# Optimization experiments

Measured on AMD Instinct MI355X. Metric: run time of the kernel, lower is better.

## Reference

```python
import jax, jax.numpy as jnp
import numpy as np

B = 32768
W = 7            # window_size (fixed: classifier head outputs 7*2 -> view(B, 7, 2))
F = 80           # per-frame feature size
WF = W * F       # window_feature_size = 560
EH = 512         # encoder_hidden_size
EO = 512         # encoder_output_size
H = 512          # core_hidden_size
NUM_STEPS = 7
EPS = 1e-5

def _linear(x, w, b):
    return x @ w.T + b

def _bn(x, g, bt, m, v):
    # BatchNorm1d in eval mode (running stats)
    return (x - m) * g / jnp.sqrt(v + EPS) + bt

def _ln(x, g, b):
    mu = x.mean(-1, keepdims=True)
    var = x.var(-1, keepdims=True)
    return (x - mu) / jnp.sqrt(var + EPS) * g + b

def setup_inputs():
    key = jax.random.key(0)
    ks = iter(jax.random.split(key, 40))
    def rn(shape, s=0.05):
        return jax.random.normal(next(ks), shape, dtype=jnp.float32) * s
    def rv(shape):
        return jax.random.uniform(next(ks), shape, dtype=jnp.float32) + 0.5
    return {
        'features': jax.random.normal(next(ks), (B, W, F), dtype=jnp.float32),
        'dec_w': rn((W, H)), 'dec_b': rn((W,)),
        'dec_bn_g': rv((W,)), 'dec_bn_b': rn((W,)), 'dec_bn_m': rn((W,)), 'dec_bn_v': rv((W,)),
        'ea1_w': rn((EH, W)), 'ea1_b': rn((EH,)),
        'ea1_bn_g': rv((EH,)), 'ea1_bn_b': rn((EH,)), 'ea1_bn_m': rn((EH,)), 'ea1_bn_v': rv((EH,)),
        'ea2_w': rn((EO, EH)), 'ea2_b': rn((EO,)),
        'ea2_bn_g': rv((EO,)), 'ea2_bn_b': rn((EO,)), 'ea2_bn_m': rn((EO,)), 'ea2_bn_v': rv((EO,)),
        'ei1_w': rn((EH, WF)), 'ei1_b': rn((EH,)),
        'ei1_bn_g': rv((EH,)), 'ei1_bn_b': rn((EH,)), 'ei1_bn_m': rn((EH,)), 'ei1_bn_v': rv((EH,)),
        'ei2_w': rn((EO, EH)), 'ei2_b': rn((EO,)),
        'ei2_bn_g': rv((EO,)), 'ei2_bn_b': rn((EO,)), 'ei2_bn_m': rn((EO,)), 'ei2_bn_v': rv((EO,)),
        'w_ih': rn((4 * H, EO)), 'w_hh': rn((4 * H, H)), 'b_ih': rn((4 * H,)), 'b_hh': rn((4 * H,)),
        'ln_g': rv((H,)), 'ln_b': rn((H,)),
        'cls_w': rn((2 * W, H)), 'cls_b': rn((2 * W,)),
    }

def _forward(features, dec_w, dec_b, dec_bn_g, dec_bn_b, dec_bn_m, dec_bn_v,
             ea1_w, ea1_b, ea1_bn_g, ea1_bn_b, ea1_bn_m, ea1_bn_v,
             ea2_w, ea2_b, ea2_bn_g, ea2_bn_b, ea2_bn_m, ea2_bn_v,
             ei1_w, ei1_b, ei1_bn_g, ei1_bn_b, ei1_bn_m, ei1_bn_v,
             ei2_w, ei2_b, ei2_bn_g, ei2_bn_b, ei2_bn_m, ei2_bn_v,
             w_ih, w_hh, b_ih, b_hh, ln_g, ln_b, cls_w, cls_b):
    Bsz = features.shape[0]

    def encoder(att):
        # attention branch: Linear -> BN -> ReLU -> Linear -> BN
        a = jax.nn.relu(_bn(_linear(att, ea1_w, ea1_b), ea1_bn_g, ea1_bn_b, ea1_bn_m, ea1_bn_v))
        a = _bn(_linear(a, ea2_w, ea2_b), ea2_bn_g, ea2_bn_b, ea2_bn_m, ea2_bn_v)
        # attended-input branch on flattened (features * att)
        ai = (features * att[:, :, None]).reshape(Bsz, WF)
        x = jax.nn.relu(_bn(_linear(ai, ei1_w, ei1_b), ei1_bn_g, ei1_bn_b, ei1_bn_m, ei1_bn_v))
        x = _bn(_linear(x, ei2_w, ei2_b), ei2_bn_g, ei2_bn_b, ei2_bn_m, ei2_bn_v)
        return jax.nn.relu(a + x)

    def lstm_step(x, h, c):
        gates = x @ w_ih.T + b_ih + h @ w_hh.T + b_hh  # [B, 4H], torch gate order i,f,g,o
        i, f, g, o = jnp.split(gates, 4, axis=-1)
        c = jax.nn.sigmoid(f) * c + jax.nn.sigmoid(i) * jnp.tanh(g)
        h = jax.nn.sigmoid(o) * jnp.tanh(c)
        return h, c

    # initial pass: uniform attention, zero LSTM state (state=None -> no LN)
    att0 = jnp.full((Bsz, W), 1.0 / W, dtype=features.dtype)
    h, c = lstm_step(encoder(att0), jnp.zeros((Bsz, H), features.dtype), jnp.zeros((Bsz, H), features.dtype))

    def body(carry, _):
        h, c = carry
        # decoder: Linear -> BN -> smooth softmax
        logits = _bn(_linear(h, dec_w, dec_b), dec_bn_g, dec_bn_b, dec_bn_m, dec_bn_v)
        s = jax.nn.sigmoid(logits)
        att = s / s.sum(-1, keepdims=True)
        agg = encoder(att)
        hn, cn = lstm_step(agg, _ln(h, ln_g, ln_b), _ln(c, ln_g, ln_b))
        return (hn, cn), None

    (h, c), _ = jax.lax.scan(body, (h, c), None, length=NUM_STEPS)
    out = _linear(h, cls_w, cls_b).reshape(Bsz, W, 2)
    return jax.nn.log_softmax(out, axis=2)

def reference(features, dec_w, dec_b, dec_bn_g, dec_bn_b, dec_bn_m, dec_bn_v,
              ea1_w, ea1_b, ea1_bn_g, ea1_bn_b, ea1_bn_m, ea1_bn_v,
              ea2_w, ea2_b, ea2_bn_g, ea2_bn_b, ea2_bn_m, ea2_bn_v,
              ei1_w, ei1_b, ei1_bn_g, ei1_bn_b, ei1_bn_m, ei1_bn_v,
              ei2_w, ei2_b, ei2_bn_g, ei2_bn_b, ei2_bn_m, ei2_bn_v,
              w_ih, w_hh, b_ih, b_hh, ln_g, ln_b, cls_w, cls_b):
    return _forward(features, dec_w, dec_b, dec_bn_g, dec_bn_b, dec_bn_m, dec_bn_v,
                    ea1_w, ea1_b, ea1_bn_g, ea1_bn_b, ea1_bn_m, ea1_bn_v,
                    ea2_w, ea2_b, ea2_bn_g, ea2_bn_b, ea2_bn_m, ea2_bn_v,
                    ei1_w, ei1_b, ei1_bn_g, ei1_bn_b, ei1_bn_m, ei1_bn_v,
                    ei2_w, ei2_b, ei2_bn_g, ei2_bn_b, ei2_bn_m, ei2_bn_v,
                    w_ih, w_hh, b_ih, b_hh, ln_g, ln_b, cls_w, cls_b)
```

## Files before the change

kernel.cpp:

```cpp
#include <hip/hip_runtime.h>
#include <cstdint>
#include <cstddef>

#define BSZ 32768
#define WN 7
#define WF 560
#define K1P 576
#define EPS 1e-5f

typedef __attribute__((ext_vector_type(8))) short bf16x8;
typedef __attribute__((ext_vector_type(4))) float f32x4;

__device__ __forceinline__ float b2f(short s) {
  union { float f; unsigned u; } x; x.u = ((unsigned)(unsigned short)s) << 16; return x.f;
}
__device__ __forceinline__ short f2b(float f) {
  union { float f; unsigned u; } x; x.f = f;
  unsigned r = x.u + 0x7fffu + ((x.u >> 16) & 1u);
  return (short)(r >> 16);
}
__device__ __forceinline__ float sigf(float x) { return 1.0f / (1.0f + __expf(-x)); }
__device__ __forceinline__ float ftanh(float x) {
  float t = __expf(-2.0f * fabsf(x));
  float r = (1.0f - t) / (1.0f + t);
  return copysignf(r, x);
}

__device__ __forceinline__ void async_copy16(const short* g, short* l) {
  __builtin_amdgcn_global_load_lds((const __attribute__((address_space(1))) unsigned*)g,
                                   (__attribute__((address_space(3))) unsigned*)l, 16, 0, 0);
}


__global__ void fold_small_k(const float* __restrict__ dec_w, const float* __restrict__ dec_b,
                             const float* __restrict__ dec_g, const float* __restrict__ dec_bt,
                             const float* __restrict__ dec_m, const float* __restrict__ dec_v,
                             const float* __restrict__ ea1_w, const float* __restrict__ ea1_b,
                             const float* __restrict__ ea1_g, const float* __restrict__ ea1_bt,
                             const float* __restrict__ ea1_m, const float* __restrict__ ea1_v,
                             float* __restrict__ decwf, float* __restrict__ decb8,
                             float* __restrict__ ea1f)
{
  int t = blockIdx.x * 256 + threadIdx.x;
  if (t < 7 * 512) {
    int w = t >> 9;
    float s = dec_g[w] * rsqrtf(dec_v[w] + EPS);
    decwf[t] = dec_w[t] * s;
  }
  if (t < 8) {
    if (t < 7) {
      float s = dec_g[t] * rsqrtf(dec_v[t] + EPS);
      decb8[t] = (dec_b[t] - dec_m[t]) * s + dec_bt[t];
    } else decb8[t] = 0.0f;
  }
  if (t < 512) {
    float s = ea1_g[t] * rsqrtf(ea1_v[t] + EPS);
    #pragma unroll
    for (int w = 0; w < 7; ++w) ea1f[t * 8 + w] = ea1_w[t * 7 + w] * s;
    ea1f[t * 8 + 7] = (ea1_b[t] - ea1_m[t]) * s + ea1_bt[t];
  }
}

__global__ void fold_ei1_k(const float* __restrict__ w, const float* __restrict__ b,
                           const float* __restrict__ g, const float* __restrict__ bt,
                           const float* __restrict__ m, const float* __restrict__ v,
                           short* __restrict__ ei1f, float* __restrict__ bias1)
{
  int idx = blockIdx.x * 256 + threadIdx.x;
  int n = idx / K1P, k = idx % K1P;
  float s = g[n] * rsqrtf(v[n] + EPS);
  ei1f[idx] = (k < WF) ? f2b(w[n * WF + k] * s) : (short)0;
  if (k == 0) bias1[n] = (b[n] - m[n]) * s + bt[n];
}

__global__ void fold_w2_k(const float* __restrict__ wi, const float* __restrict__ bi,
                          const float* __restrict__ gi, const float* __restrict__ bti,
                          const float* __restrict__ mi, const float* __restrict__ vi,
                          const float* __restrict__ wa, const float* __restrict__ ba,
                          const float* __restrict__ ga, const float* __restrict__ bta,
                          const float* __restrict__ ma, const float* __restrict__ va,
                          short* __restrict__ W2, float* __restrict__ bias2)
{
  int idx = blockIdx.x * 256 + threadIdx.x;
  int n = idx >> 10, k = idx & 1023;
  float si = gi[n] * rsqrtf(vi[n] + EPS);
  float sa = ga[n] * rsqrtf(va[n] + EPS);
  float val = (k < 512) ? wi[n * 512 + k] * si : wa[n * 512 + (k - 512)] * sa;
  W2[idx] = f2b(val);
  if (k == 0)
    bias2[n] = (bi[n] - mi[n]) * si + bti[n] + (ba[n] - ma[n]) * sa + bta[n];
}

__global__ void fold_wg_k(const float* __restrict__ w_ih, const float* __restrict__ w_hh,
                          const float* __restrict__ b_ih, const float* __restrict__ b_hh,
                          short* __restrict__ Wg, float* __restrict__ biasg)
{
  int idx = blockIdx.x * 256 + threadIdx.x;
  int c = idx >> 10, k = idx & 1023;
  int g = (c >> 4) & 3;
  int u = (c >> 6) * 16 + (c & 15);
  int r = g * 512 + u;
  float val = (k < 512) ? w_ih[r * 512 + k] : w_hh[r * 512 + (k - 512)];
  Wg[idx] = f2b(val);
  if (k == 0) biasg[c] = b_ih[r] + b_hh[r];
}

__global__ __launch_bounds__(512)
void attln_k(const float* __restrict__ hbuf, const float* __restrict__ cbuf,
             const float* __restrict__ decwf, const float* __restrict__ decb8,
             const float* __restrict__ ea1f,
             const float* __restrict__ ln_g, const float* __restrict__ ln_b,
             const float* __restrict__ feat,
             short* __restrict__ ghA, short* __restrict__ c_ln,
             short* __restrict__ xa, short* __restrict__ ai, int init)
{
  const int lane = threadIdx.x & 63;
  const int b = blockIdx.x * 8 + (threadIdx.x >> 6);
  float av[WN];
  if (init) {
    const float c7 = 1.0f / 7.0f;
    #pragma unroll
    for (int w = 0; w < WN; ++w) av[w] = c7;
    int4 z = make_int4(0, 0, 0, 0);
    *(int4*)&ghA[b * 1024 + 512 + lane * 8] = z;
    *(int4*)&c_ln[b * 512 + lane * 8] = z;
  } else {
    float hl[8];
    const float* hp = hbuf + (size_t)b * 512 + lane * 8;
    *(float4*)&hl[0] = *(const float4*)hp;
    *(float4*)&hl[4] = *(const float4*)(hp + 4);
    float s = 0.f, s2 = 0.f;
    #pragma unroll
    for (int e = 0; e < 8; ++e) { s += hl[e]; s2 += hl[e] * hl[e]; }
    float p[WN];
    #pragma unroll
    for (int w = 0; w < WN; ++w) {
      const float* dw = decwf + w * 512 + lane * 8;
      float4 w0 = *(const float4*)dw, w1 = *(const float4*)(dw + 4);
      p[w] = hl[0] * w0.x + hl[1] * w0.y + hl[2] * w0.z + hl[3] * w0.w
           + hl[4] * w1.x + hl[5] * w1.y + hl[6] * w1.z + hl[7] * w1.w;
    }
    #pragma unroll
    for (int o = 32; o > 0; o >>= 1) {
      s  += __shfl_xor(s, o);
      s2 += __shfl_xor(s2, o);
      #pragma unroll
      for (int w = 0; w < WN; ++w) p[w] += __shfl_xor(p[w], o);
    }
    float mu = s * (1.0f / 512.0f);
    float var = s2 * (1.0f / 512.0f) - mu * mu;
    float rstd = rsqrtf(var + EPS);
    float ssum = 0.f;
    #pragma unroll
    for (int w = 0; w < WN; ++w) { float sg = sigf(p[w] + decb8[w]); av[w] = sg; ssum += sg; }
    float inv = 1.0f / ssum;
    #pragma unroll
    for (int w = 0; w < WN; ++w) av[w] *= inv;
    short o8[8];
    #pragma unroll
    for (int e = 0; e < 8; ++e) {
      int i = lane * 8 + e;
      o8[e] = f2b((hl[e] - mu) * rstd * ln_g[i] + ln_b[i]);
    }
    *(int4*)&ghA[b * 1024 + 512 + lane * 8] = *(int4*)o8;
    float cl[8];
    const float* cp = cbuf + (size_t)b * 512 + lane * 8;
    *(float4*)&cl[0] = *(const float4*)cp;
    *(float4*)&cl[4] = *(const float4*)(cp + 4);
    float cs = 0.f, cs2 = 0.f;
    #pragma unroll
    for (int e = 0; e < 8; ++e) { cs += cl[e]; cs2 += cl[e] * cl[e]; }
    #pragma unroll
    for (int o = 32; o > 0; o >>= 1) {
      cs  += __shfl_xor(cs, o);
      cs2 += __shfl_xor(cs2, o);
    }
    float cmu = cs * (1.0f / 512.0f);
    float cvar = cs2 * (1.0f / 512.0f) - cmu * cmu;
    float crstd = rsqrtf(cvar + EPS);
    #pragma unroll
    for (int e = 0; e < 8; ++e) {
      int i = lane * 8 + e;
      o8[e] = f2b((cl[e] - cmu) * crstd * ln_g[i] + ln_b[i]);
    }
    *(int4*)&c_ln[b * 512 + lane * 8] = *(int4*)o8;
  }
  short a8[8];
  #pragma unroll
  for (int e = 0; e < 8; ++e) {
    int n = lane * 8 + e;
    const float* wr = ea1f + n * 8;
    float4 w0 = *(const float4*)wr, w1 = *(const float4*)(wr + 4);
    float v = w1.w
            + av[0] * w0.x + av[1] * w0.y + av[2] * w0.z + av[3] * w0.w
            + av[4] * w1.x + av[5] * w1.y + av[6] * w1.z;
    a8[e] = f2b(fmaxf(v, 0.0f));
  }
  *(int4*)&xa[b * 1024 + 512 + lane * 8] = *(int4*)a8;
  const float* fr = feat + (size_t)b * WF;
  short* air = ai + (size_t)b * K1P;
  #pragma unroll
  for (int rr = 0; rr < 2; ++rr) {
    int c8 = lane + rr * 64;
    if (c8 < 72) {
      int k = c8 * 8;
      short s8[8];
      if (k < WF) {
        int window = c8 / 10;
        float a = av[0];
        #pragma unroll
        for (int w = 1; w < WN; ++w) a = (window == w) ? av[w] : a;
        float4 f0 = *(const float4*)(fr + k);
        float4 f1 = *(const float4*)(fr + k + 4);
        s8[0] = f2b(f0.x * a); s8[1] = f2b(f0.y * a); s8[2] = f2b(f0.z * a); s8[3] = f2b(f0.w * a);
        s8[4] = f2b(f1.x * a); s8[5] = f2b(f1.y * a); s8[6] = f2b(f1.z * a); s8[7] = f2b(f1.w * a);
      } else {
        #pragma unroll
        for (int e = 0; e < 8; ++e) s8[e] = 0;
      }
      *(int4*)&air[k] = *(int4*)s8;
    }
  }
}


#define STAGE128(SRC, LD, K0, S) do {                                          \
    _Pragma("unroll")                                                          \
    for (int r_ = 0; r_ < 4; ++r_) {                                           \
      int idx_ = r_ * 256 + t;                                                 \
      int row_ = idx_ >> 3, dcol_ = (idx_ & 7) * 8;                            \
      int scol_ = dcol_ ^ ((row_ & 7) << 3);                                   \
      async_copy16(SRC + (size_t)row_ * (LD) + (K0) + scol_, &S[idx_ * 8]);    \
    }                                                                          \
  } while (0)

#define READ_FRAG(S, ROW, KS) \
  (*(const bf16x8*)&S[(ROW) * 64 + (((KS)) ^ (((ROW) & 7) << 3))])

__global__ __launch_bounds__(256)
void gemm_bt_k(const short* __restrict__ A, int lda,
               const short* __restrict__ Wt, int K,
               const float* __restrict__ bias,
               short* __restrict__ C, int ldc)
{
  __shared__ short sA[128 * 64];
  __shared__ short sB[128 * 64];
  const int t = threadIdx.x;
  const int m0 = blockIdx.x * 128;
  const int n0 = blockIdx.y * 128;
  const int wv = t >> 6, lane = t & 63;
  const int wm = (wv & 1) * 64, wn = (wv >> 1) * 64;
  const int lr = lane & 15, lk = (lane >> 4) * 8;

  f32x4 acc[4][4] = {};
  const short* Ab = A + (size_t)m0 * lda;
  const short* Wb = Wt + (size_t)n0 * K;

  for (int k0 = 0; k0 < K; k0 += 64) {
    STAGE128(Ab, lda, k0, sA);
    STAGE128(Wb, K, k0, sB);
    __syncthreads();
    #pragma unroll
    for (int ks = 0; ks < 64; ks += 32) {
      bf16x8 af[4], bfr[4];
      #pragma unroll
      for (int i = 0; i < 4; ++i) af[i]  = READ_FRAG(sA, wm + i * 16 + lr, ks + lk);
      #pragma unroll
      for (int j = 0; j < 4; ++j) bfr[j] = READ_FRAG(sB, wn + j * 16 + lr, ks + lk);
      #pragma unroll
      for (int i = 0; i < 4; ++i)
        #pragma unroll
        for (int j = 0; j < 4; ++j)
          acc[i][j] = __builtin_amdgcn_mfma_f32_16x16x32_bf16(af[i], bfr[j], acc[i][j], 0, 0, 0);
    }
    __syncthreads();
  }
  #pragma unroll
  for (int j = 0; j < 4; ++j) {
    int col = n0 + wn + j * 16 + lr;
    float bs = bias[col];
    #pragma unroll
    for (int i = 0; i < 4; ++i) {
      int rbase = m0 + wm + i * 16 + (lane >> 4) * 4;
      #pragma unroll
      for (int e = 0; e < 4; ++e) {
        float v = acc[i][j][e] + bs;
        C[(size_t)(rbase + e) * ldc + col] = f2b(fmaxf(v, 0.0f));
      }
    }
  }
}

__global__ __launch_bounds__(256)
void gates_k(const short* __restrict__ A,
             const short* __restrict__ Wg,
             const float* __restrict__ biasg,
             const short* __restrict__ c_ln,
             float* __restrict__ hbuf, float* __restrict__ cbuf)
{
  __shared__ short sA[128 * 64];
  __shared__ short sB[128 * 64];
  const int t = threadIdx.x;
  const int m0 = blockIdx.x * 128;
  const int n0 = blockIdx.y * 128;
  const int wv = t >> 6, lane = t & 63;
  const int wm = (wv & 1) * 64, wn = (wv >> 1) * 64;
  const int lr = lane & 15, lk = (lane >> 4) * 8;

  f32x4 acc[4][4] = {};
  const short* Ab = A + (size_t)m0 * 1024;
  const short* Wb = Wg + (size_t)n0 * 1024;

  for (int k0 = 0; k0 < 1024; k0 += 64) {
    STAGE128(Ab, 1024, k0, sA);
    STAGE128(Wb, 1024, k0, sB);
    __syncthreads();
    #pragma unroll
    for (int ks = 0; ks < 64; ks += 32) {
      bf16x8 af[4], bfr[4];
      #pragma unroll
      for (int i = 0; i < 4; ++i) af[i]  = READ_FRAG(sA, wm + i * 16 + lr, ks + lk);
      #pragma unroll
      for (int j = 0; j < 4; ++j) bfr[j] = READ_FRAG(sB, wn + j * 16 + lr, ks + lk);
      #pragma unroll
      for (int i = 0; i < 4; ++i)
        #pragma unroll
        for (int j = 0; j < 4; ++j)
          acc[i][j] = __builtin_amdgcn_mfma_f32_16x16x32_bf16(af[i], bfr[j], acc[i][j], 0, 0, 0);
    }
    __syncthreads();
  }
  const int u = ((n0 + wn) >> 6) * 16 + lr;
  const float bi_ = biasg[n0 + wn + 0 * 16 + lr];
  const float bf_ = biasg[n0 + wn + 1 * 16 + lr];
  const float bg_ = biasg[n0 + wn + 2 * 16 + lr];
  const float bo_ = biasg[n0 + wn + 3 * 16 + lr];
  #pragma unroll
  for (int i = 0; i < 4; ++i) {
    int rbase = m0 + wm + i * 16 + (lane >> 4) * 4;
    #pragma unroll
    for (int e = 0; e < 4; ++e) {
      int row = rbase + e;
      float iv = sigf(acc[i][0][e] + bi_);
      float fv = sigf(acc[i][1][e] + bf_);
      float gv = ftanh(acc[i][2][e] + bg_);
      float ov = sigf(acc[i][3][e] + bo_);
      float cold = b2f(c_ln[(size_t)row * 512 + u]);
      float cc = fv * cold + iv * gv;
      hbuf[(size_t)row * 512 + u] = ov * ftanh(cc);
      cbuf[(size_t)row * 512 + u] = cc;
    }
  }
}

__global__ __launch_bounds__(512)
void cls_k(const float* __restrict__ hbuf, const float* __restrict__ cw,
           const float* __restrict__ cb, float* __restrict__ out)
{
  const int lane = threadIdx.x & 63;
  const int b = blockIdx.x * 8 + (threadIdx.x >> 6);
  float hl[8];
  const float* hp = hbuf + (size_t)b * 512 + lane * 8;
  *(float4*)&hl[0] = *(const float4*)hp;
  *(float4*)&hl[4] = *(const float4*)(hp + 4);
  float p[14];
  #pragma unroll
  for (int tcol = 0; tcol < 14; ++tcol) {
    const float* wr = cw + tcol * 512 + lane * 8;
    float4 w0 = *(const float4*)wr, w1 = *(const float4*)(wr + 4);
    p[tcol] = hl[0] * w0.x + hl[1] * w0.y + hl[2] * w0.z + hl[3] * w0.w
            + hl[4] * w1.x + hl[5] * w1.y + hl[6] * w1.z + hl[7] * w1.w;
  }
  #pragma unroll
  for (int o = 32; o > 0; o >>= 1)
    #pragma unroll
    for (int tcol = 0; tcol < 14; ++tcol) p[tcol] += __shfl_xor(p[tcol], o);
  if (lane < 14) {
    float z = cb[lane];
    #pragma unroll
    for (int tcol = 0; tcol < 14; ++tcol) if (lane == tcol) z += p[tcol];
    float zp = __shfl_xor(z, 1);
    float m = fmaxf(z, zp);
    float l = m + __logf(__expf(z - m) + __expf(zp - m));
    out[(size_t)b * 14 + lane] = z - l;
  }
}


extern "C" void kernel_launch(void* const* d_in, const int* in_sizes, int n_in,
                              void* d_out, int out_size, void* d_ws, size_t ws_size,
                              hipStream_t stream)
{
  const float* features = (const float*)d_in[0];
  const float* dec_w    = (const float*)d_in[1];
  const float* dec_b    = (const float*)d_in[2];
  const float* dec_bn_g = (const float*)d_in[3];
  const float* dec_bn_b = (const float*)d_in[4];
  const float* dec_bn_m = (const float*)d_in[5];
  const float* dec_bn_v = (const float*)d_in[6];
  const float* ea1_w    = (const float*)d_in[7];
  const float* ea1_b    = (const float*)d_in[8];
  const float* ea1_bn_g = (const float*)d_in[9];
  const float* ea1_bn_b = (const float*)d_in[10];
  const float* ea1_bn_m = (const float*)d_in[11];
  const float* ea1_bn_v = (const float*)d_in[12];
  const float* ea2_w    = (const float*)d_in[13];
  const float* ea2_b    = (const float*)d_in[14];
  const float* ea2_bn_g = (const float*)d_in[15];
  const float* ea2_bn_b = (const float*)d_in[16];
  const float* ea2_bn_m = (const float*)d_in[17];
  const float* ea2_bn_v = (const float*)d_in[18];
  const float* ei1_w    = (const float*)d_in[19];
  const float* ei1_b    = (const float*)d_in[20];
  const float* ei1_bn_g = (const float*)d_in[21];
  const float* ei1_bn_b = (const float*)d_in[22];
  const float* ei1_bn_m = (const float*)d_in[23];
  const float* ei1_bn_v = (const float*)d_in[24];
  const float* ei2_w    = (const float*)d_in[25];
  const float* ei2_b    = (const float*)d_in[26];
  const float* ei2_bn_g = (const float*)d_in[27];
  const float* ei2_bn_b = (const float*)d_in[28];
  const float* ei2_bn_m = (const float*)d_in[29];
  const float* ei2_bn_v = (const float*)d_in[30];
  const float* w_ih     = (const float*)d_in[31];
  const float* w_hh     = (const float*)d_in[32];
  const float* b_ih     = (const float*)d_in[33];
  const float* b_hh     = (const float*)d_in[34];
  const float* ln_g     = (const float*)d_in[35];
  const float* ln_b     = (const float*)d_in[36];
  const float* cls_w    = (const float*)d_in[37];
  const float* cls_b    = (const float*)d_in[38];
  (void)in_sizes; (void)n_in; (void)out_size;

  int chunk = BSZ;
  while (chunk > 2048 && (size_t)chunk * 10368 + (16u << 20) > ws_size) chunk >>= 1;

  char* ws = (char*)d_ws;
  size_t off = 0;
  auto carve = [&](size_t bytes) -> void* {
    void* p = ws + off;
    off += (bytes + 255) & ~(size_t)255;
    return p;
  };
  short* ei1f  = (short*)carve((size_t)512 * K1P * 2);
  float* bias1 = (float*)carve(512 * 4);
  short* W2    = (short*)carve((size_t)512 * 1024 * 2);
  float* bias2 = (float*)carve(512 * 4);
  short* Wg    = (short*)carve((size_t)2048 * 1024 * 2);
  float* biasg = (float*)carve(2048 * 4);
  float* decwf = (float*)carve(7 * 512 * 4);
  float* decb8 = (float*)carve(8 * 4);
  float* ea1f  = (float*)carve(512 * 8 * 4);
  float* hbuf  = (float*)carve((size_t)chunk * 512 * 4);
  float* cbuf  = (float*)carve((size_t)chunk * 512 * 4);
  short* ghA   = (short*)carve((size_t)chunk * 1024 * 2);
  short* xa    = (short*)carve((size_t)chunk * 1024 * 2);
  short* clnb  = (short*)carve((size_t)chunk * 512 * 2);
  short* ai    = (short*)carve((size_t)chunk * K1P * 2);

  fold_small_k<<<16, 256, 0, stream>>>(dec_w, dec_b, dec_bn_g, dec_bn_b, dec_bn_m, dec_bn_v,
                                       ea1_w, ea1_b, ea1_bn_g, ea1_bn_b, ea1_bn_m, ea1_bn_v,
                                       decwf, decb8, ea1f);
  fold_ei1_k<<<(512 * K1P) / 256, 256, 0, stream>>>(ei1_w, ei1_b, ei1_bn_g, ei1_bn_b,
                                                    ei1_bn_m, ei1_bn_v, ei1f, bias1);
  fold_w2_k<<<(512 * 1024) / 256, 256, 0, stream>>>(ei2_w, ei2_b, ei2_bn_g, ei2_bn_b, ei2_bn_m, ei2_bn_v,
                                                    ea2_w, ea2_b, ea2_bn_g, ea2_bn_b, ea2_bn_m, ea2_bn_v,
                                                    W2, bias2);
  fold_wg_k<<<(2048 * 1024) / 256, 256, 0, stream>>>(w_ih, w_hh, b_ih, b_hh, Wg, biasg);

  for (int base = 0; base < BSZ; base += chunk) {
    const float* featc = features + (size_t)base * WF;
    float* outc = (float*)d_out + (size_t)base * 14;
    for (int s = 0; s < 8; ++s) {
      attln_k<<<chunk / 8, 512, 0, stream>>>(hbuf, cbuf, decwf, decb8, ea1f, ln_g, ln_b,
                                             featc, ghA, clnb, xa, ai, (s == 0) ? 1 : 0);
      gemm_bt_k<<<dim3(chunk / 128, 4), 256, 0, stream>>>(ai, K1P, ei1f, K1P, bias1, xa, 1024);
      gemm_bt_k<<<dim3(chunk / 128, 4), 256, 0, stream>>>(xa, 1024, W2, 1024, bias2, ghA, 1024);
      gates_k<<<dim3(chunk / 128, 16), 256, 0, stream>>>(ghA, Wg, biasg, clnb, hbuf, cbuf);
    }
    cls_k<<<chunk / 8, 512, 0, stream>>>(hbuf, cls_w, cls_b, outc);
  }
}
```

Baseline: 3.065 ms.

## Triple-buffer gates GEMM with async prefetch and larger 256x128 tiles

Rewrites the LSTM gates GEMM kernel to use 512-thread blocks covering 256x128 output tiles. Operands are staged through a three-deep LDS ring with async copies issued two K-steps ahead, synchronised by vmcnt waits and a single barrier per step. MFMA sections run at raised wave priority. The aim is to hide global-load latency and drop the double __syncthreads per K-step. In exchange, LDS use rises to roughly 144KB per block, which limits occupancy, and correctness depends on the hand-tuned waitcnt counts.

```diff
diff --git a/kernel.cpp b/kernel.cpp
--- a/kernel.cpp
+++ b/kernel.cpp
@@ -223,7 +223,6 @@
   }
 }
 
-
 #define STAGE128(SRC, LD, K0, S) do {                                          \
     _Pragma("unroll")                                                          \
     for (int r_ = 0; r_ < 4; ++r_) {                                           \
@@ -291,60 +290,104 @@
   }
 }
 
-__global__ __launch_bounds__(256)
+
+#define G_STAGE(g) do {                                                              \
+    short* dA_ = &sA[((g) % 3) * 16384];                                             \
+    short* dB_ = &sB[((g) % 3) * 8192];                                              \
+    _Pragma("unroll")                                                                \
+    for (int q_ = 0; q_ < 4; ++q_) {                                                 \
+      int idx_ = q_ * 512 + t;                                                       \
+      int row_ = idx_ >> 3, ds_ = idx_ & 7;                                          \
+      int sc_ = (ds_ ^ (row_ & 7)) * 8;                                              \
+      async_copy16(A + (size_t)(m0 + row_) * 1024 + (g) * 64 + sc_, dA_ + idx_ * 8); \
+    }                                                                                \
+    _Pragma("unroll")                                                                \
+    for (int q_ = 0; q_ < 2; ++q_) {                                                 \
+      int idx_ = q_ * 512 + t;                                                       \
+      int row_ = idx_ >> 3, ds_ = idx_ & 7;                                          \
+      int sc_ = (ds_ ^ (row_ & 7)) * 8;                                              \
+      async_copy16(Wg + (size_t)(n0 + row_) * 1024 + (g) * 64 + sc_, dB_ + idx_ * 8);\
+    }                                                                                \
+  } while (0)
+
+#define G_COMPUTE(g) do {                                                            \
+    const short* bA_ = &sA[((g) % 3) * 16384];                                       \
+    const short* bB_ = &sB[((g) % 3) * 8192];                                        \
+    bf16x8 af_[4][2], bf_[4][2];                                                     \
+    _Pragma("unroll")                                                                \
+    for (int mf_ = 0; mf_ < 4; ++mf_) {                                              \
+      int row_ = wm * 64 + mf_ * 16 + lr;                                            \
+      _Pragma("unroll")                                                              \
+      for (int ks_ = 0; ks_ < 2; ++ks_)                                              \
+        af_[mf_][ks_] = *(const bf16x8*)&bA_[row_ * 64 + (((ks_ * 4 + hi) ^ (row_ & 7)) * 8)]; \
+    }                                                                                \
+    _Pragma("unroll")                                                                \
+    for (int nf_ = 0; nf_ < 4; ++nf_) {                                              \
+      int row_ = wn * 64 + nf_ * 16 + lr;                                            \
+      _Pragma("unroll")                                                              \
+      for (int ks_ = 0; ks_ < 2; ++ks_)                                              \
+        bf_[nf_][ks_] = *(const bf16x8*)&bB_[row_ * 64 + (((ks_ * 4 + hi) ^ (row_ & 7)) * 8)]; \
+    }                                                                                \
+    __builtin_amdgcn_s_setprio(1);                                                   \
+    _Pragma("unroll")                                                                \
+    for (int mf_ = 0; mf_ < 4; ++mf_)                                                \
+      _Pragma("unroll")                                                              \
+      for (int nf_ = 0; nf_ < 4; ++nf_) {                                            \
+        acc[mf_][nf_] = __builtin_amdgcn_mfma_f32_16x16x32_bf16(af_[mf_][0], bf_[nf_][0], acc[mf_][nf_], 0, 0, 0); \
+        acc[mf_][nf_] = __builtin_amdgcn_mfma_f32_16x16x32_bf16(af_[mf_][1], bf_[nf_][1], acc[mf_][nf_], 0, 0, 0); \
+      }                                                                              \
+    __builtin_amdgcn_s_setprio(0);                                                   \
+  } while (0)
+
+__global__ __launch_bounds__(512, 2)
 void gates_k(const short* __restrict__ A,
              const short* __restrict__ Wg,
              const float* __restrict__ biasg,
              const short* __restrict__ c_ln,
              float* __restrict__ hbuf, float* __restrict__ cbuf)
 {
-  __shared__ short sA[128 * 64];
-  __shared__ short sB[128 * 64];
+  __shared__ short sA[3 * 256 * 64];
+  __shared__ short sB[3 * 128 * 64];
   const int t = threadIdx.x;
-  const int m0 = blockIdx.x * 128;
+  const int m0 = blockIdx.x * 256;
   const int n0 = blockIdx.y * 128;
-  const int wv = t >> 6, lane = t & 63;
-  const int wm = (wv & 1) * 64, wn = (wv >> 1) * 64;
-  const int lr = lane & 15, lk = (lane >> 4) * 8;
+  const int wid = t >> 6, lane = t & 63;
+  const int wm = wid >> 1, wn = wid & 1;
+  const int lr = lane & 15, hi = lane >> 4;
 
   f32x4 acc[4][4] = {};
-  const short* Ab = A + (size_t)m0 * 1024;
-  const short* Wb = Wg + (size_t)n0 * 1024;
-
-  for (int k0 = 0; k0 < 1024; k0 += 64) {
-    STAGE128(Ab, 1024, k0, sA);
-    STAGE128(Wb, 1024, k0, sB);
-    __syncthreads();
-    #pragma unroll
-    for (int ks = 0; ks < 64; ks += 32) {
-      bf16x8 af[4], bfr[4];
-      #pragma unroll
-      for (int i = 0; i < 4; ++i) af[i]  = READ_FRAG(sA, wm + i * 16 + lr, ks + lk);
-      #pragma unroll
-      for (int j = 0; j < 4; ++j) bfr[j] = READ_FRAG(sB, wn + j * 16 + lr, ks + lk);
-      #pragma unroll
-      for (int i = 0; i < 4; ++i)
-        #pragma unroll
-        for (int j = 0; j < 4; ++j)
-          acc[i][j] = __builtin_amdgcn_mfma_f32_16x16x32_bf16(af[i], bfr[j], acc[i][j], 0, 0, 0);
-    }
-    __syncthreads();
-  }
-  const int u = ((n0 + wn) >> 6) * 16 + lr;
-  const float bi_ = biasg[n0 + wn + 0 * 16 + lr];
-  const float bf_ = biasg[n0 + wn + 1 * 16 + lr];
-  const float bg_ = biasg[n0 + wn + 2 * 16 + lr];
-  const float bo_ = biasg[n0 + wn + 3 * 16 + lr];
-  #pragma unroll
-  for (int i = 0; i < 4; ++i) {
-    int rbase = m0 + wm + i * 16 + (lane >> 4) * 4;
+
+  G_STAGE(0);
+  G_STAGE(1);
+  asm volatile("s_waitcnt vmcnt(6)" ::: "memory");
+  __builtin_amdgcn_s_barrier();
+
+  #pragma unroll
+  for (int g = 0; g < 16; ++g) {
+    if (g + 2 < 16) G_STAGE(g + 2);
+    G_COMPUTE(g);
+    if (g < 14)
+      asm volatile("s_waitcnt vmcnt(6) lgkmcnt(0)" ::: "memory");
+    else if (g == 14)
+      asm volatile("s_waitcnt vmcnt(0) lgkmcnt(0)" ::: "memory");
+    if (g < 15) __builtin_amdgcn_s_barrier();
+  }
+
+  const int u = ((n0 + wn * 64) >> 6) * 16 + lr;
+  const float bi_ = biasg[n0 + wn * 64 + 0 * 16 + lr];
+  const float bf2 = biasg[n0 + wn * 64 + 1 * 16 + lr];
+  const float bg_ = biasg[n0 + wn * 64 + 2 * 16 + lr];
+  const float bo_ = biasg[n0 + wn * 64 + 3 * 16 + lr];
+  #pragma unroll
+  for (int mf = 0; mf < 4; ++mf) {
+    int rbase = m0 + wm * 64 + mf * 16 + hi * 4;
     #pragma unroll
     for (int e = 0; e < 4; ++e) {
       int row = rbase + e;
-      float iv = sigf(acc[i][0][e] + bi_);
-      float fv = sigf(acc[i][1][e] + bf_);
-      float gv = ftanh(acc[i][2][e] + bg_);
-      float ov = sigf(acc[i][3][e] + bo_);
+      float iv = sigf(acc[mf][0][e] + bi_);
+      float fv = sigf(acc[mf][1][e] + bf2);
+      float gv = ftanh(acc[mf][2][e] + bg_);
+      float ov = sigf(acc[mf][3][e] + bo_);
       float cold = b2f(c_ln[(size_t)row * 512 + u]);
       float cc = fv * cold + iv * gv;
       hbuf[(size_t)row * 512 + u] = ov * ftanh(cc);
@@ -476,7 +519,7 @@
                                              featc, ghA, clnb, xa, ai, (s == 0) ? 1 : 0);
       gemm_bt_k<<<dim3(chunk / 128, 4), 256, 0, stream>>>(ai, K1P, ei1f, K1P, bias1, xa, 1024);
       gemm_bt_k<<<dim3(chunk / 128, 4), 256, 0, stream>>>(xa, 1024, W2, 1024, bias2, ghA, 1024);
-      gates_k<<<dim3(chunk / 128, 16), 256, 0, stream>>>(ghA, Wg, biasg, clnb, hbuf, cbuf);
+      gates_k<<<dim3(chunk / 256, 16), 512, 0, stream>>>(ghA, Wg, biasg, clnb, hbuf, cbuf);
     }
     cls_k<<<chunk / 8, 512, 0, stream>>>(hbuf, cls_w, cls_b, outc);
   }
```

Measured after the change: 2.829 ms. 1.08x faster.
